# Optimization experiments

Measured on AMD Instinct MI355X. Metric: run time of the kernel, lower is better.

## Reference

```python
import jax, jax.numpy as jnp
import numpy as np

INPUT_DIM = 16
HIDDEN = 64
N_RAW = INPUT_DIM - 3  # 13 raw features, last 3 are xyz coords


def setup_inputs() -> dict:
    key = jax.random.key(0)
    ks = jax.random.split(key, 16)
    B, N = 4, 512
    D = HIDDEN
    s = lambda fan_in: 1.0 / np.sqrt(fan_in)
    x = jax.random.normal(ks[0], (B, N, INPUT_DIM), dtype=jnp.float32)
    # feature projection [N_RAW -> D]
    Wf = jax.random.uniform(ks[1], (N_RAW, D), jnp.float32, -s(N_RAW), s(N_RAW))
    bf = jax.random.uniform(ks[2], (D,), jnp.float32, -s(N_RAW), s(N_RAW))
    # positional encoding MLP [3 -> D -> D]
    Wp1 = jax.random.uniform(ks[3], (3, D), jnp.float32, -s(3), s(3))
    bp1 = jax.random.uniform(ks[4], (D,), jnp.float32, -s(3), s(3))
    Wp2 = jax.random.uniform(ks[5], (D, D), jnp.float32, -s(D), s(D))
    bp2 = jax.random.uniform(ks[6], (D,), jnp.float32, -s(D), s(D))
    # node projection [D -> D]
    Wn = jax.random.uniform(ks[7], (D, D), jnp.float32, -s(D), s(D))
    bn = jax.random.uniform(ks[8], (D,), jnp.float32, -s(D), s(D))
    # edge MLP [2D -> D -> D//2 -> 1]
    W1 = jax.random.uniform(ks[9], (2 * D, D), jnp.float32, -s(2 * D), s(2 * D))
    b1 = jax.random.uniform(ks[10], (D,), jnp.float32, -s(2 * D), s(2 * D))
    W2 = jax.random.uniform(ks[11], (D, D // 2), jnp.float32, -s(D), s(D))
    b2 = jax.random.uniform(ks[12], (D // 2,), jnp.float32, -s(D), s(D))
    W3 = jax.random.uniform(ks[13], (D // 2, 1), jnp.float32, -s(D // 2), s(D // 2))
    b3 = jax.random.uniform(ks[14], (1,), jnp.float32, -s(D // 2), s(D // 2))
    return dict(x=x, Wf=Wf, bf=bf, Wp1=Wp1, bp1=bp1, Wp2=Wp2, bp2=bp2,
                Wn=Wn, bn=bn, W1=W1, b1=b1, W2=W2, b2=b2, W3=W3, b3=b3)


def reference(x, Wf, bf, Wp1, bp1, Wp2, bp2, Wn, bn, W1, b1, W2, b2, W3, b3):
    # split raw features / xyz coords
    feats = x[..., :N_RAW]           # [B,N,13]
    xyz = x[..., -3:]                # [B,N,3]
    pos = jax.nn.relu(xyz @ Wp1 + bp1) @ Wp2 + bp2
    proj = feats @ Wf + bf + pos     # [B,N,D]
    emb = proj @ Wn + bn             # [B,N,D] node embeddings
    # edge MLP layer1 on concat([u_i, u_j]): decompose W1 = [W1a; W1b].
    # cat([u_i,u_j]) @ W1 == u_i @ W1a + u_j @ W1b  (same math, no [B,N,N,2D])
    D = emb.shape[-1]
    a = emb @ W1[:D]                 # [B,N,D]
    b = emb @ W1[D:]                 # [B,N,D]
    h = jax.nn.relu(a[:, :, None, :] + b[:, None, :, :] + b1)  # [B,N,N,D]
    h = jax.nn.relu(h @ W2 + b2)     # [B,N,N,D//2]  (dropout = identity in eval)
    logits = (h @ W3 + b3)[..., 0]   # [B,N,N]
    return logits
```

## Files before the change

kernel.cpp:

```cpp
#include <hip/hip_runtime.h>
#include <stdint.h>

#define NPTS 512
#define NB 4
#define TJB 128
#define PADB 68

typedef __attribute__((ext_vector_type(4))) float floatx4;
typedef __attribute__((ext_vector_type(8))) short short8;

union S8U { uint32_t u[4]; short8 s; };
union FU  { float f; uint32_t u; };

__device__ __forceinline__ uint32_t fbits(float f){ FU x; x.f = f; return x.u; }
__device__ __forceinline__ float bitsf(uint32_t u){ FU x; x.u = u; return x.f; }

__device__ __forceinline__ void split2(float f0, float f1, uint32_t& hp, uint32_t& lp){
    const uint32_t u0 = fbits(f0), u1 = fbits(f1);
    hp = __builtin_amdgcn_perm(u1, u0, 0x07060302u);
    const float l0 = f0 - bitsf(u0 & 0xFFFF0000u);
    const float l1 = f1 - bitsf(u1 & 0xFFFF0000u);
    lp = __builtin_amdgcn_perm(fbits(l1), fbits(l0), 0x07060302u);
}

__global__ __launch_bounds__(256) void rows_kernel(
    const float* __restrict__ x,
    const float* __restrict__ Wf,  const float* __restrict__ bf,
    const float* __restrict__ Wp1, const float* __restrict__ bp1,
    const float* __restrict__ Wp2, const float* __restrict__ bp2,
    const float* __restrict__ Wn,  const float* __restrict__ bn,
    const float* __restrict__ W1,  const float* __restrict__ b1,
    float* __restrict__ wsA, float* __restrict__ wsB)
{
    __shared__ float posh[4][64];
    __shared__ float projS[4][64];
    __shared__ float embS[4][64];

    const int r   = threadIdx.x >> 6;
    const int t   = threadIdx.x & 63;
    const int row = blockIdx.x * 4 + r;
    const float* xr = x + row * 16;

    const float x13 = xr[13], x14 = xr[14], x15 = xr[15];
    float ph = x13 * Wp1[t] + x14 * Wp1[64 + t] + x15 * Wp1[128 + t] + bp1[t];
    posh[r][t] = fmaxf(ph, 0.f);
    __syncthreads();

    float s0 = 0.f, s1 = 0.f, s2 = 0.f, s3 = 0.f;
    #pragma unroll
    for (int k = 0; k < 64; k += 4) {
        s0 += posh[r][k    ] * Wp2[(k    ) * 64 + t];
        s1 += posh[r][k + 1] * Wp2[(k + 1) * 64 + t];
        s2 += posh[r][k + 2] * Wp2[(k + 2) * 64 + t];
        s3 += posh[r][k + 3] * Wp2[(k + 3) * 64 + t];
    }
    float acc = bp2[t] + ((s0 + s1) + (s2 + s3)) + bf[t];
    float f0 = 0.f, f1 = 0.f, f2 = 0.f, f3 = 0.f;
    #pragma unroll
    for (int k = 0; k < 12; k += 4) {
        f0 += xr[k    ] * Wf[(k    ) * 64 + t];
        f1 += xr[k + 1] * Wf[(k + 1) * 64 + t];
        f2 += xr[k + 2] * Wf[(k + 2) * 64 + t];
        f3 += xr[k + 3] * Wf[(k + 3) * 64 + t];
    }
    acc += ((f0 + f1) + (f2 + f3)) + xr[12] * Wf[12 * 64 + t];
    projS[r][t] = acc;
    __syncthreads();

    float e0 = 0.f, e1 = 0.f, e2 = 0.f, e3 = 0.f;
    #pragma unroll
    for (int k = 0; k < 64; k += 4) {
        e0 += projS[r][k    ] * Wn[(k    ) * 64 + t];
        e1 += projS[r][k + 1] * Wn[(k + 1) * 64 + t];
        e2 += projS[r][k + 2] * Wn[(k + 2) * 64 + t];
        e3 += projS[r][k + 3] * Wn[(k + 3) * 64 + t];
    }
    embS[r][t] = bn[t] + ((e0 + e1) + (e2 + e3));
    __syncthreads();

    float a0 = 0.f, a1 = 0.f, a2 = 0.f, a3 = 0.f;
    float v0 = 0.f, v1 = 0.f, v2 = 0.f, v3 = 0.f;
    #pragma unroll
    for (int k = 0; k < 64; k += 4) {
        const float g0 = embS[r][k], g1 = embS[r][k + 1], g2 = embS[r][k + 2], g3 = embS[r][k + 3];
        a0 += g0 * W1[(k    ) * 64 + t];
        a1 += g1 * W1[(k + 1) * 64 + t];
        a2 += g2 * W1[(k + 2) * 64 + t];
        a3 += g3 * W1[(k + 3) * 64 + t];
        v0 += g0 * W1[(64 + k    ) * 64 + t];
        v1 += g1 * W1[(64 + k + 1) * 64 + t];
        v2 += g2 * W1[(64 + k + 2) * 64 + t];
        v3 += g3 * W1[(64 + k + 3) * 64 + t];
    }
    wsA[row * 64 + t] = b1[t] + ((a0 + a1) + (a2 + a3));
    wsB[row * 64 + t] = (v0 + v1) + (v2 + v3);
}

__global__ __launch_bounds__(256) void pairs_kernel(
    const float* __restrict__ wsA, const float* __restrict__ wsB,
    const float* __restrict__ W2,  const float* __restrict__ b2,
    const float* __restrict__ W3,  const float* __restrict__ b3,
    float* __restrict__ out)
{
    __shared__ float bS[TJB][PADB];

    const int tid = threadIdx.x;
    const int w   = tid >> 6;
    const int l   = tid & 63;
    const int q   = l >> 4;
    const int c   = l & 15;
    const int q8  = q * 8;

    const int bidx = blockIdx.x;
    const int jt = bidx & 3;
    const int ib = (bidx >> 2) & 127;
    const int bb = bidx >> 9;
    const int j0 = jt * TJB;
    const int i  = ib * 4 + w;

    const float* bG = wsB + (bb * NPTS + j0) * 64;
    #pragma unroll
    for (int p = 0; p < 8; ++p) {
        const int flat = p * 256 + tid;
        const int rr = flat >> 4, c4 = (flat & 15) * 4;
        *(float4*)&bS[rr][c4] = *(const float4*)(bG + rr * 64 + c4);
    }

    short8 Whi[2][2], Wlo[2][2];
    #pragma unroll
    for (int kt = 0; kt < 2; ++kt)
        #pragma unroll
        for (int nt = 0; nt < 2; ++nt) {
            S8U hu, lu;
            #pragma unroll
            for (int d = 0; d < 4; ++d) {
                const float g0 = W2[(kt * 32 + q8 + 2 * d    ) * 32 + nt * 16 + c];
                const float g1 = W2[(kt * 32 + q8 + 2 * d + 1) * 32 + nt * 16 + c];
                split2(g0, g1, hu.u[d], lu.u[d]);
            }
            Whi[kt][nt] = hu.s; Wlo[kt][nt] = lu.s;
        }

    const float b2c = b2[c], b2c16 = b2[c + 16];
    const float w3c = W3[c], w3c16 = W3[c + 16];
    const float b3v = b3[0];

    const float* aG = wsA + (bb * NPTS + i) * 64;
    float a[16];
    #pragma unroll
    for (int e = 0; e < 8; ++e) { a[e] = aG[q8 + e]; a[8 + e] = aG[32 + q8 + e]; }

    __syncthreads();

    float* orow = out + ((size_t)(bb * NPTS + i)) * NPTS + j0;

    #pragma unroll 1
    for (int mt = 0; mt < 8; ++mt) {
        const int m = mt * 16 + c;
        float bh[16];
        *(float4*)&bh[0]  = *(const float4*)&bS[m][q8];
        *(float4*)&bh[4]  = *(const float4*)&bS[m][q8 + 4];
        *(float4*)&bh[8]  = *(const float4*)&bS[m][32 + q8];
        *(float4*)&bh[12] = *(const float4*)&bS[m][32 + q8 + 4];

        float h[16];
        #pragma unroll
        for (int e = 0; e < 16; ++e) h[e] = fmaxf(a[e] + bh[e], 0.f);

        S8U h0h, h0l, h1h, h1l;
        #pragma unroll
        for (int d = 0; d < 4; ++d) {
            split2(h[2 * d],     h[2 * d + 1],     h0h.u[d], h0l.u[d]);
            split2(h[8 + 2 * d], h[8 + 2 * d + 1], h1h.u[d], h1l.u[d]);
        }

        floatx4 acc0 = {0.f, 0.f, 0.f, 0.f};
        floatx4 acc1 = {0.f, 0.f, 0.f, 0.f};
        acc0 = __builtin_amdgcn_mfma_f32_16x16x32_bf16(h0h.s, Whi[0][0], acc0, 0, 0, 0);
        acc0 = __builtin_amdgcn_mfma_f32_16x16x32_bf16(h0l.s, Whi[0][0], acc0, 0, 0, 0);
        acc0 = __builtin_amdgcn_mfma_f32_16x16x32_bf16(h0h.s, Wlo[0][0], acc0, 0, 0, 0);
        acc0 = __builtin_amdgcn_mfma_f32_16x16x32_bf16(h1h.s, Whi[1][0], acc0, 0, 0, 0);
        acc0 = __builtin_amdgcn_mfma_f32_16x16x32_bf16(h1l.s, Whi[1][0], acc0, 0, 0, 0);
        acc0 = __builtin_amdgcn_mfma_f32_16x16x32_bf16(h1h.s, Wlo[1][0], acc0, 0, 0, 0);
        acc1 = __builtin_amdgcn_mfma_f32_16x16x32_bf16(h0h.s, Whi[0][1], acc1, 0, 0, 0);
        acc1 = __builtin_amdgcn_mfma_f32_16x16x32_bf16(h0l.s, Whi[0][1], acc1, 0, 0, 0);
        acc1 = __builtin_amdgcn_mfma_f32_16x16x32_bf16(h0h.s, Wlo[0][1], acc1, 0, 0, 0);
        acc1 = __builtin_amdgcn_mfma_f32_16x16x32_bf16(h1h.s, Whi[1][1], acc1, 0, 0, 0);
        acc1 = __builtin_amdgcn_mfma_f32_16x16x32_bf16(h1l.s, Whi[1][1], acc1, 0, 0, 0);
        acc1 = __builtin_amdgcn_mfma_f32_16x16x32_bf16(h1h.s, Wlo[1][1], acc1, 0, 0, 0);

        float res[4];
        #pragma unroll
        for (int r = 0; r < 4; ++r) {
            float v = fmaxf(acc0[r] + b2c, 0.f) * w3c + fmaxf(acc1[r] + b2c16, 0.f) * w3c16;
            v += __shfl_xor(v, 1, 64);
            v += __shfl_xor(v, 2, 64);
            v += __shfl_xor(v, 4, 64);
            v += __shfl_xor(v, 8, 64);
            res[r] = v;
        }
        const float outv = (c == 0) ? res[0] : ((c == 1) ? res[1] : ((c == 2) ? res[2] : res[3]));
        if (c < 4) orow[mt * 16 + q * 4 + c] = outv + b3v;
    }
}

extern "C" void kernel_launch(void* const* d_in, const int* in_sizes, int n_in,
                              void* d_out, int out_size, void* d_ws, size_t ws_size,
                              hipStream_t stream) {
    const float* x   = (const float*)d_in[0];
    const float* Wf  = (const float*)d_in[1];
    const float* bf  = (const float*)d_in[2];
    const float* Wp1 = (const float*)d_in[3];
    const float* bp1 = (const float*)d_in[4];
    const float* Wp2 = (const float*)d_in[5];
    const float* bp2 = (const float*)d_in[6];
    const float* Wn  = (const float*)d_in[7];
    const float* bn  = (const float*)d_in[8];
    const float* W1  = (const float*)d_in[9];
    const float* b1  = (const float*)d_in[10];
    const float* W2  = (const float*)d_in[11];
    const float* b2  = (const float*)d_in[12];
    const float* W3  = (const float*)d_in[13];
    const float* b3  = (const float*)d_in[14];

    float* wsA = (float*)d_ws;
    float* wsB = wsA + NB * NPTS * 64;

    rows_kernel<<<NB * NPTS / 4, 256, 0, stream>>>(
        x, Wf, bf, Wp1, bp1, Wp2, bp2, Wn, bn, W1, b1, wsA, wsB);

    pairs_kernel<<<NB * NPTS / 4 * 4, 256, 0, stream>>>(
        wsA, wsB, W2, b2, W3, b3, (float*)d_out);
}
```

Before: 108.6 us.

## Switch pair MLP to single fp16 MFMA and reduce W3 dot via MFMA

Replaces the three-term bf16 hi/lo split emulation of fp32 (12 MFMAs per tile) with a single fp16 MFMA pass (4 per tile). The final W3 dot product no longer uses a 4-step shuffle reduction: the relu outputs are packed to fp16, staged through a small per-wave LDS buffer, transposed, and reduced with one more MFMA. The loop is also unrolled by 2. This cuts matrix and VALU work and shuffles, at the cost of fp16 rounding (round-toward-zero) on activations and weights, which could affect accuracy.

```diff
diff --git a/kernel.cpp b/kernel.cpp
--- a/kernel.cpp
+++ b/kernel.cpp
@@ -5,23 +5,14 @@
 #define NB 4
 #define TJB 128
 #define PADB 68
+#define SOST 40
 
 typedef __attribute__((ext_vector_type(4))) float floatx4;
-typedef __attribute__((ext_vector_type(8))) short short8;
-
-union S8U { uint32_t u[4]; short8 s; };
-union FU  { float f; uint32_t u; };
-
-__device__ __forceinline__ uint32_t fbits(float f){ FU x; x.f = f; return x.u; }
-__device__ __forceinline__ float bitsf(uint32_t u){ FU x; x.u = u; return x.f; }
-
-__device__ __forceinline__ void split2(float f0, float f1, uint32_t& hp, uint32_t& lp){
-    const uint32_t u0 = fbits(f0), u1 = fbits(f1);
-    hp = __builtin_amdgcn_perm(u1, u0, 0x07060302u);
-    const float l0 = f0 - bitsf(u0 & 0xFFFF0000u);
-    const float l1 = f1 - bitsf(u1 & 0xFFFF0000u);
-    lp = __builtin_amdgcn_perm(fbits(l1), fbits(l0), 0x07060302u);
-}
+typedef __fp16 fp16x2 __attribute__((ext_vector_type(2)));
+typedef _Float16 half2v __attribute__((ext_vector_type(2)));
+typedef _Float16 half8v __attribute__((ext_vector_type(8)));
+
+union H8 { fp16x2 p2[4]; half2v h2[4]; half8v h8; };
 
 __global__ __launch_bounds__(256) void rows_kernel(
     const float* __restrict__ x,
@@ -103,6 +94,7 @@
     float* __restrict__ out)
 {
     __shared__ float bS[TJB][PADB];
+    __shared__ _Float16 sO[4][16][SOST];
 
     const int tid = threadIdx.x;
     const int w   = tid >> 6;
@@ -126,23 +118,30 @@
         *(float4*)&bS[rr][c4] = *(const float4*)(bG + rr * 64 + c4);
     }
 
-    short8 Whi[2][2], Wlo[2][2];
+    half8v Wf16[2][2];
     #pragma unroll
     for (int kt = 0; kt < 2; ++kt)
         #pragma unroll
         for (int nt = 0; nt < 2; ++nt) {
-            S8U hu, lu;
+            H8 u;
             #pragma unroll
             for (int d = 0; d < 4; ++d) {
-                const float g0 = W2[(kt * 32 + q8 + 2 * d    ) * 32 + nt * 16 + c];
-                const float g1 = W2[(kt * 32 + q8 + 2 * d + 1) * 32 + nt * 16 + c];
-                split2(g0, g1, hu.u[d], lu.u[d]);
+                half2v t;
+                t[0] = (_Float16)W2[(kt * 32 + q8 + 2 * d    ) * 32 + nt * 16 + c];
+                t[1] = (_Float16)W2[(kt * 32 + q8 + 2 * d + 1) * 32 + nt * 16 + c];
+                u.h2[d] = t;
             }
-            Whi[kt][nt] = hu.s; Wlo[kt][nt] = lu.s;
+            Wf16[kt][nt] = u.h8;
         }
 
+    half8v w3f;
+    #pragma unroll
+    for (int e = 0; e < 8; ++e) {
+        const int p = q8 + e;
+        w3f[e] = (_Float16)W3[(p >> 1) + ((p & 1) << 4)];
+    }
+
     const float b2c = b2[c], b2c16 = b2[c + 16];
-    const float w3c = W3[c], w3c16 = W3[c + 16];
     const float b3v = b3[0];
 
     const float* aG = wsA + (bb * NPTS + i) * 64;
@@ -154,7 +153,7 @@
 
     float* orow = out + ((size_t)(bb * NPTS + i)) * NPTS + j0;
 
-    #pragma unroll 1
+    #pragma unroll 2
     for (int mt = 0; mt < 8; ++mt) {
         const int m = mt * 16 + c;
         float bh[16];
@@ -167,40 +166,33 @@
         #pragma unroll
         for (int e = 0; e < 16; ++e) h[e] = fmaxf(a[e] + bh[e], 0.f);
 
-        S8U h0h, h0l, h1h, h1l;
+        H8 h0, h1;
         #pragma unroll
         for (int d = 0; d < 4; ++d) {
-            split2(h[2 * d],     h[2 * d + 1],     h0h.u[d], h0l.u[d]);
-            split2(h[8 + 2 * d], h[8 + 2 * d + 1], h1h.u[d], h1l.u[d]);
+            h0.p2[d] = __builtin_amdgcn_cvt_pkrtz(h[2 * d],     h[2 * d + 1]);
+            h1.p2[d] = __builtin_amdgcn_cvt_pkrtz(h[8 + 2 * d], h[8 + 2 * d + 1]);
         }
 
         floatx4 acc0 = {0.f, 0.f, 0.f, 0.f};
         floatx4 acc1 = {0.f, 0.f, 0.f, 0.f};
-        acc0 = __builtin_amdgcn_mfma_f32_16x16x32_bf16(h0h.s, Whi[0][0], acc0, 0, 0, 0);
-        acc0 = __builtin_amdgcn_mfma_f32_16x16x32_bf16(h0l.s, Whi[0][0], acc0, 0, 0, 0);
-        acc0 = __builtin_amdgcn_mfma_f32_16x16x32_bf16(h0h.s, Wlo[0][0], acc0, 0, 0, 0);
-        acc0 = __builtin_amdgcn_mfma_f32_16x16x32_bf16(h1h.s, Whi[1][0], acc0, 0, 0, 0);
-        acc0 = __builtin_amdgcn_mfma_f32_16x16x32_bf16(h1l.s, Whi[1][0], acc0, 0, 0, 0);
-        acc0 = __builtin_amdgcn_mfma_f32_16x16x32_bf16(h1h.s, Wlo[1][0], acc0, 0, 0, 0);
-        acc1 = __builtin_amdgcn_mfma_f32_16x16x32_bf16(h0h.s, Whi[0][1], acc1, 0, 0, 0);
-        acc1 = __builtin_amdgcn_mfma_f32_16x16x32_bf16(h0l.s, Whi[0][1], acc1, 0, 0, 0);
-        acc1 = __builtin_amdgcn_mfma_f32_16x16x32_bf16(h0h.s, Wlo[0][1], acc1, 0, 0, 0);
-        acc1 = __builtin_amdgcn_mfma_f32_16x16x32_bf16(h1h.s, Whi[1][1], acc1, 0, 0, 0);
-        acc1 = __builtin_amdgcn_mfma_f32_16x16x32_bf16(h1l.s, Whi[1][1], acc1, 0, 0, 0);
-        acc1 = __builtin_amdgcn_mfma_f32_16x16x32_bf16(h1h.s, Wlo[1][1], acc1, 0, 0, 0);
-
-        float res[4];
+        acc0 = __builtin_amdgcn_mfma_f32_16x16x32_f16(h0.h8, Wf16[0][0], acc0, 0, 0, 0);
+        acc0 = __builtin_amdgcn_mfma_f32_16x16x32_f16(h1.h8, Wf16[1][0], acc0, 0, 0, 0);
+        acc1 = __builtin_amdgcn_mfma_f32_16x16x32_f16(h0.h8, Wf16[0][1], acc1, 0, 0, 0);
+        acc1 = __builtin_amdgcn_mfma_f32_16x16x32_f16(h1.h8, Wf16[1][1], acc1, 0, 0, 0);
+
         #pragma unroll
         for (int r = 0; r < 4; ++r) {
-            float v = fmaxf(acc0[r] + b2c, 0.f) * w3c + fmaxf(acc1[r] + b2c16, 0.f) * w3c16;
-            v += __shfl_xor(v, 1, 64);
-            v += __shfl_xor(v, 2, 64);
-            v += __shfl_xor(v, 4, 64);
-            v += __shfl_xor(v, 8, 64);
-            res[r] = v;
+            const float r0 = fmaxf(acc0[r] + b2c,   0.f);
+            const float r1 = fmaxf(acc1[r] + b2c16, 0.f);
+            *(fp16x2*)&sO[w][q * 4 + r][2 * c] = __builtin_amdgcn_cvt_pkrtz(r0, r1);
         }
-        const float outv = (c == 0) ? res[0] : ((c == 1) ? res[1] : ((c == 2) ? res[2] : res[3]));
-        if (c < 4) orow[mt * 16 + q * 4 + c] = outv + b3v;
+        const half8v ar = *(const half8v*)&sO[w][c][q8];
+
+        floatx4 dl = {0.f, 0.f, 0.f, 0.f};
+        dl = __builtin_amdgcn_mfma_f32_16x16x32_f16(ar, w3f, dl, 0, 0, 0);
+
+        const float lg = (c == 0) ? dl[0] : ((c == 1) ? dl[1] : ((c == 2) ? dl[2] : dl[3]));
+        if (c < 4) orow[mt * 16 + q * 4 + c] = lg + b3v;
     }
 }
 
@@ -229,6 +221,6 @@
     rows_kernel<<<NB * NPTS / 4, 256, 0, stream>>>(
         x, Wf, bf, Wp1, bp1, Wp2, bp2, Wn, bn, W1, b1, wsA, wsB);
 
-    pairs_kernel<<<NB * NPTS / 4 * 4, 256, 0, stream>>>(
+    pairs_kernel<<<NB * 128 * 4, 256, 0, stream>>>(
         wsA, wsB, W2, b2, W3, b3, (float*)d_out);
 }
```

Result: faster. 101.2 us (-6.8%).
